# Kernel tuning notes

Measured on AMD Instinct MI355X. Metric: run time of the kernel, lower is better.

The kernel has to match this reference:

```python
import jax, jax.numpy as jnp
import numpy as np

STRIDE = 1
PAD = (1, 1)  # (padding_h, padding_w)


def setup_inputs() -> dict:
    key = jax.random.key(0)
    k1, k2, k3, k4 = jax.random.split(key, 4)
    # 8-bit activation / weight codes (indices into the 256x256 LUT)
    input = jax.random.randint(k1, (8, 64, 56, 56), 0, 256, dtype=jnp.int32)
    weight = jax.random.randint(k2, (128, 64, 3, 3), 0, 256, dtype=jnp.int32)
    # LUT holds the approximate products lut[a, w]; float32 so accumulation is fp32
    lut = jax.random.normal(k3, (256, 256), dtype=jnp.float32)
    bias = jax.random.normal(k4, (128,), dtype=jnp.float32)
    return {"input": input, "weight": weight, "lut": lut, "bias": bias}


def _extract_patches(x, K, stride, ph, pw, OH, OW):
    # im2col with (ci, kh, kw) flattening order to match weight.reshape(Cout, -1)
    xp = jnp.pad(x, ((0, 0), (0, 0), (ph, ph), (pw, pw)))
    pat = jnp.stack(
        [xp[:, :, kh:kh + stride * OH:stride, kw:kw + stride * OW:stride]
         for kh in range(K) for kw in range(K)],
        axis=2,
    )  # [B, Cin, K*K, OH, OW]
    B, Cin = x.shape[0], x.shape[1]
    return pat.reshape(B, Cin * K * K, OH, OW)


def reference(input, weight, lut, bias):
    B, Cin, H, W = input.shape
    Cout, _, K, _ = weight.shape
    stride, (ph, pw) = STRIDE, PAD
    OH = (H + 2 * ph - K) // stride + 1
    OW = (W + 2 * pw - K) // stride + 1
    L = Cin * K * K  # reduction length per output element

    patches = _extract_patches(input, K, stride, ph, pw, OH, OW)  # [B, L, OH, OW] int
    wflat = weight.reshape(Cout, L)                                # [Cout, L] int

    # Pre-gather LUT rows per (output-channel, tap): T[l, a, co] = lut[a, weight[co, l]]
    T = jnp.transpose(lut[:, wflat], (2, 0, 1))  # [L, 256, Cout] float32
    idx = jnp.transpose(patches, (1, 0, 2, 3))   # [L, B, OH, OW]

    def body(acc, xs):
        i, t = xs            # i: [B, OH, OW] int, t: [256, Cout]
        return acc + t[i], None  # gather per tap, accumulate in fp32

    acc0 = jnp.zeros((B, OH, OW, Cout), jnp.float32)
    acc, _ = jax.lax.scan(body, acc0, (idx, T))

    out = jnp.transpose(acc, (0, 3, 1, 2)) + bias[None, :, None, None]
    return out
```

## Files before the change

kernel.cpp:

```cpp
#include <hip/hip_runtime.h>

#define CIN   64
#define COUT  128
#define HW    56
#define LTAPS 576


__global__ __launch_bounds__(1024) void lut_absmax(const float* __restrict__ lut,
                                                   float* __restrict__ ws_scale) {
    __shared__ float red[16];
    int tid = threadIdx.x;
    float m = 0.f;
    const float4* l4 = (const float4*)lut;
    for (int i = tid; i < 16384; i += 1024) {
        float4 v = l4[i];
        m = fmaxf(m, fmaxf(fmaxf(fabsf(v.x), fabsf(v.y)),
                           fmaxf(fabsf(v.z), fabsf(v.w))));
    }
    for (int off = 32; off > 0; off >>= 1)
        m = fmaxf(m, __shfl_down(m, off, 64));
    if ((tid & 63) == 0) red[tid >> 6] = m;
    __syncthreads();
    if (tid == 0) {
#pragma unroll
        for (int i = 1; i < 16; ++i) m = fmaxf(m, red[i]);
        ws_scale[0] = m / 127.0f;
    }
}

__global__ __launch_bounds__(256) void transpose_w(const int* __restrict__ weight,
                                                   int* __restrict__ wT) {
    int idx = blockIdx.x * 256 + threadIdx.x;
    wT[idx] = weight[(idx & 127) * LTAPS + (idx >> 7)];
}

__global__ __launch_bounds__(256) void build_G8(const int* __restrict__ wT,
                                                const float* __restrict__ lut,
                                                const float* __restrict__ ws_scale,
                                                uint2* __restrict__ G) {
    int idx = blockIdx.x * 256 + threadIdx.x;
    int c8 = idx & 15;
    int la = idx >> 4;
    int a  = la & 255;
    int l  = la >> 8;
    int co = c8 * 8;
    float inv = 1.0f / ws_scale[0];
    const float* lr = lut + a * 256;
    const int*   wr = wT + l * 128 + co;
    int4 wa = *(const int4*)wr;
    int4 wb = *(const int4*)(wr + 4);
    int w[8] = {wa.x, wa.y, wa.z, wa.w, wb.x, wb.y, wb.z, wb.w};
    unsigned int p0 = 0, p1 = 0;
#pragma unroll
    for (int j = 0; j < 4; ++j) {
        int qv = (int)rintf(lr[w[j]] * inv) + 128;
        qv = qv < 0 ? 0 : (qv > 255 ? 255 : qv);
        p0 |= (unsigned int)qv << (8 * j);
    }
#pragma unroll
    for (int j = 0; j < 4; ++j) {
        int qv = (int)rintf(lr[w[4 + j]] * inv) + 128;
        qv = qv < 0 ? 0 : (qv > 255 ? 255 : qv);
        p1 |= (unsigned int)qv << (8 * j);
    }
    uint2 v; v.x = p0; v.y = p1;
    G[idx] = v;
}


#if __has_builtin(__builtin_amdgcn_perm)
#define ODDB(w) __builtin_amdgcn_perm(0u, (w), 0x0C030C01u)
#else
#define ODDB(w) (((w) >> 8) & 0x00FF00FFu)
#endif

#define MACC4(w, L, H)  L += (w) & 0x00FF00FFu;  H += ODDB(w);

#define MACC16(d)                                                              \
    MACC4((d).x, aL0, aH0) MACC4((d).y, aL1, aH1)                              \
    MACC4((d).z, aL2, aH2) MACC4((d).w, aL3, aH3)

#define DECL3(p) uint4 p##0, p##1, p##2;

#define PF3(p, ci, ky)                                                         \
    {                                                                          \
        const unsigned char* sc = sA + (ci) * 24 + pb + (ky) * 6;              \
        const unsigned char* Gl = Gq + ((size_t)((ci) * 9 + (ky) * 3) << 15);  \
        p##0 = *(const uint4*)(Gl + (0 << 15) + ((int)sc[0] << 7));            \
        p##1 = *(const uint4*)(Gl + (1 << 15) + ((int)sc[1] << 7));            \
        p##2 = *(const uint4*)(Gl + (2 << 15) + ((int)sc[2] << 7));            \
    }

#define CS3(p) MACC16(p##0) MACC16(p##1) MACC16(p##2)

#define FLUSH16                                                                \
    A0  += aL0 & 0xFFFFu;  A2  += aL0 >> 16;                                   \
    A1  += aH0 & 0xFFFFu;  A3  += aH0 >> 16;                                   \
    A4  += aL1 & 0xFFFFu;  A6  += aL1 >> 16;                                   \
    A5  += aH1 & 0xFFFFu;  A7  += aH1 >> 16;                                   \
    A8  += aL2 & 0xFFFFu;  A10 += aL2 >> 16;                                   \
    A9  += aH2 & 0xFFFFu;  A11 += aH2 >> 16;                                   \
    A12 += aL3 & 0xFFFFu;  A14 += aL3 >> 16;                                   \
    A13 += aH3 & 0xFFFFu;  A15 += aH3 >> 16;                                   \
    aL0 = aL1 = aL2 = aL3 = 0u; aH0 = aH1 = aH2 = aH3 = 0u;

__global__ __launch_bounds__(64) void conv_i8(const int* __restrict__ input,
                                              const unsigned char* __restrict__ G,
                                              const float* __restrict__ bias,
                                              const float* __restrict__ ws_scale,
                                              float* __restrict__ out) {
    __shared__ unsigned char sA[CIN * 24];

    int bx = blockIdx.x;
    int b  = bx / 392;
    int r  = bx % 392;
    int y0 = (r / 14) * 2;
    int x0 = (r % 14) * 4;

    int tid = threadIdx.x;

    for (int i = tid; i < CIN * 24; i += 64) {
        int ci = i / 24, rr = i % 24;
        int yy = y0 + rr / 6 - 1;
        int xx = x0 + rr % 6 - 1;
        int v = 0;
        if (yy >= 0 && yy < HW && xx >= 0 && xx < HW)
            v = input[((b * CIN + ci) * HW + yy) * HW + xx];
        sA[i] = (unsigned char)v;
    }
    __syncthreads();

    const int q  = tid & 7;
    const int g  = tid >> 3;
    const int py = g >> 2, px = g & 3;
    const int pb = py * 6 + px;
    const unsigned char* Gq = G + q * 16;

    unsigned int A0  = 0, A1  = 0, A2  = 0, A3  = 0;
    unsigned int A4  = 0, A5  = 0, A6  = 0, A7  = 0;
    unsigned int A8  = 0, A9  = 0, A10 = 0, A11 = 0;
    unsigned int A12 = 0, A13 = 0, A14 = 0, A15 = 0;
    unsigned int aL0 = 0, aL1 = 0, aL2 = 0, aL3 = 0;
    unsigned int aH0 = 0, aH1 = 0, aH2 = 0, aH3 = 0;

    DECL3(u)
    DECL3(v)
    PF3(u, 0, 0);

    for (int ci0 = 0; ci0 < CIN; ci0 += 2) {
        PF3(v, ci0, 1);       CS3(u)
        PF3(u, ci0, 2);       CS3(v)
        PF3(v, ci0 + 1, 0);   CS3(u)
        PF3(u, ci0 + 1, 1);   CS3(v)
        PF3(v, ci0 + 1, 2);   CS3(u)
        if (ci0 + 2 < CIN) { PF3(u, ci0 + 2, 0); }
        CS3(v)
        if (((ci0 + 2) & 15) == 0) { FLUSH16 }
    }

    const float s   = ws_scale[0];
    const int   oh  = y0 + py, ow = x0 + px;
    const int   cob = q * 16;
    const float* bb = bias + cob;
    float* ob = out + (size_t)(b * COUT + cob) * (HW * HW)
                    + (size_t)oh * HW + ow;
    ob[0  * HW * HW] = s * (float)((int)A0  - 73728) + bb[0];
    ob[1  * HW * HW] = s * (float)((int)A1  - 73728) + bb[1];
    ob[2  * HW * HW] = s * (float)((int)A2  - 73728) + bb[2];
    ob[3  * HW * HW] = s * (float)((int)A3  - 73728) + bb[3];
    ob[4  * HW * HW] = s * (float)((int)A4  - 73728) + bb[4];
    ob[5  * HW * HW] = s * (float)((int)A5  - 73728) + bb[5];
    ob[6  * HW * HW] = s * (float)((int)A6  - 73728) + bb[6];
    ob[7  * HW * HW] = s * (float)((int)A7  - 73728) + bb[7];
    ob[8  * HW * HW] = s * (float)((int)A8  - 73728) + bb[8];
    ob[9  * HW * HW] = s * (float)((int)A9  - 73728) + bb[9];
    ob[10 * HW * HW] = s * (float)((int)A10 - 73728) + bb[10];
    ob[11 * HW * HW] = s * (float)((int)A11 - 73728) + bb[11];
    ob[12 * HW * HW] = s * (float)((int)A12 - 73728) + bb[12];
    ob[13 * HW * HW] = s * (float)((int)A13 - 73728) + bb[13];
    ob[14 * HW * HW] = s * (float)((int)A14 - 73728) + bb[14];
    ob[15 * HW * HW] = s * (float)((int)A15 - 73728) + bb[15];
}

__global__ __launch_bounds__(256) void conv_direct(const int* __restrict__ input,
                                                   const int* __restrict__ weight,
                                                   const float* __restrict__ lut,
                                                   const float* __restrict__ bias,
                                                   float* __restrict__ out) {
    __shared__ unsigned char sA[CIN * 36];

    int bx = blockIdx.x;
    int b  = bx / 196;
    int r  = bx % 196;
    int y0 = (r / 14) * 4;
    int x0 = (r % 14) * 4;

    int tid = threadIdx.x;
    for (int i = tid; i < CIN * 36; i += 256) {
        int ci = i / 36, rr = i % 36;
        int yy = y0 + rr / 6 - 1;
        int xx = x0 + rr % 6 - 1;
        int v = 0;
        if (yy >= 0 && yy < HW && xx >= 0 && xx < HW)
            v = input[((b * CIN + ci) * HW + yy) * HW + xx];
        sA[i] = (unsigned char)v;
    }
    __syncthreads();

    const int q  = tid & 31;
    const int g  = tid >> 5;
    const int qv = q * 4;
    const int p0 = g * 2, p1 = p0 + 1;
    const int py0 = p0 >> 2, px0 = p0 & 3;
    const int py1 = p1 >> 2, px1 = p1 & 3;
    const int pb0 = py0 * 6 + px0;
    const int pb1 = py1 * 6 + px1;

    float acc0[4] = {0.f, 0.f, 0.f, 0.f};
    float acc1[4] = {0.f, 0.f, 0.f, 0.f};
    const int off[9] = {0, 1, 2, 6, 7, 8, 12, 13, 14};

    for (int ci = 0; ci < CIN; ++ci) {
        const int cbase = ci * 36;
#pragma unroll
        for (int t = 0; t < 9; ++t) {
            const int l = ci * 9 + t;
            const int a0 = sA[cbase + pb0 + off[t]];
            const int a1 = sA[cbase + pb1 + off[t]];
#pragma unroll
            for (int j = 0; j < 4; ++j) {
                const int w = weight[(qv + j) * LTAPS + l];
                acc0[j] += lut[a0 * 256 + w];
                acc1[j] += lut[a1 * 256 + w];
            }
        }
    }

    const int oh0 = y0 + py0, ow0 = x0 + px0;
    const int oh1 = y0 + py1, ow1 = x0 + px1;
#pragma unroll
    for (int j = 0; j < 4; ++j) {
        const int co = qv + j;
        const float bb = bias[co];
        out[((size_t)(b * COUT + co) * HW + oh0) * HW + ow0] = acc0[j] + bb;
        out[((size_t)(b * COUT + co) * HW + oh1) * HW + ow1] = acc1[j] + bb;
    }
}

extern "C" void kernel_launch(void* const* d_in, const int* in_sizes, int n_in,
                              void* d_out, int out_size, void* d_ws, size_t ws_size,
                              hipStream_t stream) {
    const int*   input  = (const int*)d_in[0];
    const int*   weight = (const int*)d_in[1];
    const float* lut    = (const float*)d_in[2];
    const float* bias   = (const float*)d_in[3];
    float*       out    = (float*)d_out;

    const size_t g_off  = 256;
    const size_t g_size = (size_t)LTAPS * 256 * 128;
    const size_t w_off  = g_off + g_size;
    const size_t need   = w_off + (size_t)LTAPS * 128 * 4;

    if (ws_size >= need) {
        float*         ws_scale = (float*)d_ws;
        unsigned char* G        = (unsigned char*)d_ws + g_off;
        int*           wT       = (int*)((unsigned char*)d_ws + w_off);
        lut_absmax<<<1, 1024, 0, stream>>>(lut, ws_scale);
        transpose_w<<<LTAPS * 128 / 256, 256, 0, stream>>>(weight, wT);
        build_G8<<<LTAPS * 16, 256, 0, stream>>>(wT, lut, ws_scale, (uint2*)G);
        conv_i8<<<8 * 392, 64, 0, stream>>>(input, G, bias, ws_scale, out);
    } else {
        conv_direct<<<8 * 196, 256, 0, stream>>>(input, weight, lut, bias, out);
    }
}
```

Baseline: 145.2 us.

## Quantize transposed LUT once and build gather table from LDS-resident copy

Replaces the weight-transpose and per-entry LUT quantize/gather kernels with two kernels. The first quantizes the whole LUT to bytes once, stored transposed. The second loads that 64 KB table into shared memory per tap and assembles the packed 8-bit G rows with byte gathers from LDS. This removes repeated global float gathers and repeated quantization when building G, at the cost of a full 64 KB LDS fill per block, which limits occupancy to one block per CU.

```diff
diff --git a/kernel.cpp b/kernel.cpp
--- a/kernel.cpp
+++ b/kernel.cpp
@@ -28,43 +28,53 @@
     }
 }
 
-__global__ __launch_bounds__(256) void transpose_w(const int* __restrict__ weight,
-                                                   int* __restrict__ wT) {
+__global__ __launch_bounds__(256) void quant_lutT(const float* __restrict__ lut,
+                                                  const float* __restrict__ ws_scale,
+                                                  unsigned char* __restrict__ luqT) {
     int idx = blockIdx.x * 256 + threadIdx.x;
-    wT[idx] = weight[(idx & 127) * LTAPS + (idx >> 7)];
-}
-
-__global__ __launch_bounds__(256) void build_G8(const int* __restrict__ wT,
-                                                const float* __restrict__ lut,
-                                                const float* __restrict__ ws_scale,
-                                                uint2* __restrict__ G) {
-    int idx = blockIdx.x * 256 + threadIdx.x;
-    int c8 = idx & 15;
-    int la = idx >> 4;
-    int a  = la & 255;
-    int l  = la >> 8;
-    int co = c8 * 8;
+    int a = idx & 255;
+    int w = idx >> 8;
     float inv = 1.0f / ws_scale[0];
-    const float* lr = lut + a * 256;
-    const int*   wr = wT + l * 128 + co;
-    int4 wa = *(const int4*)wr;
-    int4 wb = *(const int4*)(wr + 4);
-    int w[8] = {wa.x, wa.y, wa.z, wa.w, wb.x, wb.y, wb.z, wb.w};
-    unsigned int p0 = 0, p1 = 0;
-#pragma unroll
-    for (int j = 0; j < 4; ++j) {
-        int qv = (int)rintf(lr[w[j]] * inv) + 128;
-        qv = qv < 0 ? 0 : (qv > 255 ? 255 : qv);
-        p0 |= (unsigned int)qv << (8 * j);
-    }
-#pragma unroll
-    for (int j = 0; j < 4; ++j) {
-        int qv = (int)rintf(lr[w[4 + j]] * inv) + 128;
-        qv = qv < 0 ? 0 : (qv > 255 ? 255 : qv);
-        p1 |= (unsigned int)qv << (8 * j);
-    }
-    uint2 v; v.x = p0; v.y = p1;
-    G[idx] = v;
+    int qv = (int)rintf(lut[a * 256 + w] * inv) + 128;
+    qv = qv < 0 ? 0 : (qv > 255 ? 255 : qv);
+    luqT[idx] = (unsigned char)qv;
+}
+
+__global__ __launch_bounds__(256) void build_G8_lds(const int* __restrict__ weight,
+                                                    const unsigned char* __restrict__ luqT,
+                                                    uint4* __restrict__ G) {
+    __shared__ unsigned char sluq[65536];
+    __shared__ int sw[128];
+
+    const int l = blockIdx.x;
+    const int tid = threadIdx.x;
+
+    {
+        uint4* d = (uint4*)sluq;
+        const uint4* ssrc = (const uint4*)luqT;
+        for (int i = tid; i < 4096; i += 256) d[i] = ssrc[i];
+    }
+    if (tid < 128) sw[tid] = weight[tid * LTAPS + l];
+    __syncthreads();
+
+    const int a = tid;
+    uint4* grow = G + ((size_t)(l * 256 + a) << 3);
+#pragma unroll
+    for (int j = 0; j < 8; ++j) {
+        unsigned int wds[4];
+#pragma unroll
+        for (int k = 0; k < 4; ++k) {
+            const int cb = j * 16 + k * 4;
+            unsigned int x = 0;
+            x |= (unsigned int)sluq[sw[cb + 0] * 256 + a];
+            x |= (unsigned int)sluq[sw[cb + 1] * 256 + a] << 8;
+            x |= (unsigned int)sluq[sw[cb + 2] * 256 + a] << 16;
+            x |= (unsigned int)sluq[sw[cb + 3] * 256 + a] << 24;
+            wds[k] = x;
+        }
+        uint4 o; o.x = wds[0]; o.y = wds[1]; o.z = wds[2]; o.w = wds[3];
+        grow[j] = o;
+    }
 }
 
 
@@ -258,16 +268,16 @@
 
     const size_t g_off  = 256;
     const size_t g_size = (size_t)LTAPS * 256 * 128;
-    const size_t w_off  = g_off + g_size;
-    const size_t need   = w_off + (size_t)LTAPS * 128 * 4;
+    const size_t q_off  = g_off + g_size;
+    const size_t need   = q_off + 65536;
 
     if (ws_size >= need) {
         float*         ws_scale = (float*)d_ws;
         unsigned char* G        = (unsigned char*)d_ws + g_off;
-        int*           wT       = (int*)((unsigned char*)d_ws + w_off);
+        unsigned char* luqT     = (unsigned char*)d_ws + q_off;
         lut_absmax<<<1, 1024, 0, stream>>>(lut, ws_scale);
-        transpose_w<<<LTAPS * 128 / 256, 256, 0, stream>>>(weight, wT);
-        build_G8<<<LTAPS * 16, 256, 0, stream>>>(wT, lut, ws_scale, (uint2*)G);
+        quant_lutT<<<256, 256, 0, stream>>>(lut, ws_scale, luqT);
+        build_G8_lds<<<LTAPS, 256, 0, stream>>>(weight, luqT, (uint4*)G);
         conv_i8<<<8 * 392, 64, 0, stream>>>(input, G, bias, ws_scale, out);
     } else {
         conv_direct<<<8 * 196, 256, 0, stream>>>(input, weight, lut, bias, out);
```

Measured after the change: 141.9 us. 1.02x faster.
